# Kernel tuning notes

Hardware: AMD Instinct MI355X
Metric: run time of the kernel (lower is better)

Reference implementation:

```python
import jax, jax.numpy as jnp
import numpy as np

V, E, H, T, B = 10004, 96, 670, 20, 256


def setup_inputs() -> dict:
    key = jax.random.key(0)
    ks = iter(jax.random.split(key, 48))
    def p(*shape):
        return jax.random.normal(next(ks), shape, jnp.float32) * 0.05
    emb = p(V, E).at[0].set(0.0)  # padding_idx=0 row zeroed
    return dict(
        x=jax.random.randint(next(ks), (B, T), 0, V, jnp.int32),
        emb=emb,
        g_wi=p(4 * H, E), g_wh=p(4 * H, H), g_bi=p(4 * H), g_bh=p(4 * H),
        l_wi=p(4 * H, E), l_wh=p(4 * H, H), l_bi=p(4 * H), l_bh=p(4 * H),
        gl1_w=p(E, H), gl1_b=p(E), ll1_w=p(E, H), ll1_b=p(E),
        gl2_w=p(V, E), gl2_b=p(V), ll2_w=p(V, E), ll2_b=p(V),
        p1_w=p(500, E + 2 * H), p1_b=p(500),
        p2_w=p(250, 500), p2_b=p(250),
        p3_w=p(100, 250), p3_b=p(100),
        p4_w=p(50, 100), p4_b=p(50),
        pe_w=p(2, 50), pe_b=p(2),
        q1_w=p(75, 192), q1_b=p(75),
        q2_w=p(30, 75), q2_b=p(30),
        q2e_w=p(2, 30), q2e_b=p(2),
        q3_w=p(10, 30), q3_b=p(10),
        q3e_w=p(2, 10), q3e_b=p(2),
    )


def _lstm(x, h, c, wi, wh, bi, bh):
    # torch.nn.LSTMCell gate order: i, f, g, o
    g = x @ wi.T + bi + h @ wh.T + bh
    i, f, gg, o = jnp.split(g, 4, axis=-1)
    c = jax.nn.sigmoid(f) * c + jax.nn.sigmoid(i) * jnp.tanh(gg)
    h = jax.nn.sigmoid(o) * jnp.tanh(c)
    return h, c


def reference(x, emb, g_wi, g_wh, g_bi, g_bh, l_wi, l_wh, l_bi, l_bh,
              gl1_w, gl1_b, ll1_w, ll1_b, gl2_w, gl2_b, ll2_w, ll2_b,
              p1_w, p1_b, p2_w, p2_b, p3_w, p3_b, p4_w, p4_b, pe_w, pe_b,
              q1_w, q1_b, q2_w, q2_b, q2e_w, q2e_b, q3_w, q3_b, q3e_w, q3e_b):
    relu = jax.nn.relu
    embs = emb[x]                      # [B,T,E]
    Bb, Tt = x.shape
    Hh = g_wh.shape[1]
    z0 = jnp.zeros((Bb, Hh), embs.dtype)

    def step(carry, e_t):
        gh, gc, lh, lc = carry
        gh, gc = _lstm(e_t, gh, gc, g_wi, g_wh, g_bi, g_bh)
        lh, lc = _lstm(e_t, lh, lc, l_wi, l_wh, l_bi, l_bh)
        h = relu(jnp.concatenate([e_t, gh, lh], 1) @ p1_w.T + p1_b)
        h = relu(h @ p2_w.T + p2_b)
        h = relu(h @ p3_w.T + p3_b)
        h = relu(h @ p4_w.T + p4_b)
        prob = jax.nn.softmax(h @ pe_w.T + pe_b, axis=1)  # [B,2]
        # bmm([B,1,2],[B,2,H]) with tilde=[local, global]
        ghm = prob[:, 0:1] * lh + prob[:, 1:2] * gh
        gcm = prob[:, 0:1] * lc + prob[:, 1:2] * gc
        return (ghm, gcm, lh, lc), (ghm, prob)

    _, (hs, probs) = jax.lax.scan(step, (z0, z0, z0, z0), jnp.swapaxes(embs, 0, 1))
    hidden_states = jnp.swapaxes(hs, 0, 1)    # [B,T,H]
    probs_loop = jnp.swapaxes(probs, 0, 1)    # [B,T,2]

    global_x = hidden_states @ gl1_w.T + gl1_b  # [B,T,E]
    local_x = hidden_states @ ll1_w.T + ll1_b   # [B,T,E]
    sf = jnp.concatenate([global_x, local_x], -1)  # [B,T,192]
    h = relu(sf @ q1_w.T + q1_b)
    h = relu(h @ q2_w.T + q2_b)
    y = relu(h @ q2e_w.T + q2e_b)               # p1 logits [B,T,2]
    h2 = relu(h @ q3_w.T + q3_b)
    zz = relu(h2 @ q3e_w.T + q3e_b)             # p2 logits [B,T,2]

    p1s = jax.nn.softmax(y, axis=2)
    ph = jnp.broadcast_to(probs_loop[:, :, None, :], (Bb, Tt, Tt, 2))  # repeat(1,1,T,1)
    ph = jnp.concatenate([ph, p1s[:, None, :, :]], axis=1)
    xm = p1s[:, :, 0:1] * global_x + p1s[:, :, 1:2] * local_x
    gl = xm @ gl2_w.T + gl2_b                   # [B,T,V]
    ll = xm @ ll2_w.T + ll2_b
    p2s = jax.nn.softmax(zz, axis=2)
    ph = jnp.concatenate([ph, p2s[:, None, :, :]], axis=1)  # [B,T+2,T,2]
    logits = gl * p2s[:, :, 0:1] + ll * p2s[:, :, 1:2]
    return jnp.transpose(logits, (0, 2, 1)), ph
```

## Files before the change

### kernel.cpp

```cpp
#include <hip/hip_runtime.h>

#define DI __device__ __forceinline__

typedef unsigned short u16;
typedef unsigned int u32;
typedef __bf16 bf16x8 __attribute__((ext_vector_type(8)));
typedef float f32x4 __attribute__((ext_vector_type(4)));

static constexpr int B = 256, Tn = 20, En = 96, Hn = 670, Vn = 10004;
static constexpr int HP = 672;

DI float bf2f(u16 u) { union { u32 i; float f; } v; v.i = ((u32)u) << 16; return v.f; }
DI u16 f2bf(float f) {
    u32 u = __float_as_uint(f);
    u32 r = (u + 0x7FFFu + ((u >> 16) & 1u)) >> 16;
    return (u16)r;
}
DI float sigm(float x) { return 1.f / (1.f + __expf(-x)); }
DI float tanha(float x) {
    x = fminf(fmaxf(x, -15.f), 15.f);
    float e = __expf(2.f * x);
    return (e - 1.f) / (e + 1.f);
}
DI bf16x8 frag(const u16* p) { return *(const bf16x8*)p; }
DI f32x4 mfma16(bf16x8 a, bf16x8 b, f32x4 c) {
    return __builtin_amdgcn_mfma_f32_16x16x32_bf16(a, b, c, 0, 0, 0);
}
DI u16 ldw(const u16* src, long long i, int f) {
    return f ? f2bf(((const float*)src)[i]) : src[i];
}
DI float ldf(const u16* src, long long i, int f) {
    return f ? ((const float*)src)[i] : bf2f(src[i]);
}

struct Ptrs {
    const int* x;
    const u16 *emb, *g_wi, *g_wh, *g_bi, *g_bh, *l_wi, *l_wh, *l_bi, *l_bh;
    const u16 *gl1_w, *gl1_b, *ll1_w, *ll1_b, *gl2_w, *gl2_b, *ll2_w, *ll2_b;
    const u16 *p1_w, *p1_b, *p2_w, *p2_b, *p3_w, *p3_b, *p4_w, *p4_b, *pe_w, *pe_b;
    const u16 *q1_w, *q1_b, *q2_w, *q2_b, *q2e_w, *q2e_b, *q3_w, *q3_b, *q3e_w, *q3e_b;
    int  *flagp;
    u16 *embs;
    u16 *WgCat;
    u16 *P1W;
    u16 *W1C;
    u16 *W2C;
    float *BSUM;
    u16 *hs;
    u16 *hcat;
    u16 *uw;
    float *ghf, *gcf, *lhf, *lc2, *gcm;
    float *L1out;
    float *sf;
    float *p2sbuf;
    u16 *n_p1b, *n_p2w, *n_p2b, *n_p3w, *n_p3b, *n_p4w, *n_p4b, *n_pew, *n_peb;
    u16 *n_gl1b, *n_ll1b, *n_gl2b, *n_ll2b;
    u16 *n_q1w, *n_q1b, *n_q2w, *n_q2b, *n_q2ew, *n_q2eb, *n_q3w, *n_q3b, *n_q3ew, *n_q3eb;
    u16 *out0, *out1;
    float *out0f, *out1f;
};

__global__ __launch_bounds__(64) void k_detect(Ptrs p) {
    int lane = threadIdx.x;
    u32 d = ((const u32*)p.g_bi)[lane];
    u16 lo = (u16)(d & 0xffffu);
    int e = (lo >> 7) & 0xff;
    unsigned long long m = __ballot(e >= 127);
    if (lane == 0) p.flagp[0] = (m != 0ull) ? 1 : 0;
}

__global__ __launch_bounds__(256) void k_norm(Ptrs p) {
    const int f = p.flagp[0];
    int i = blockIdx.x * 256 + threadIdx.x;
    const u16* srcs[23] = {p.p1_b, p.p2_w, p.p2_b, p.p3_w, p.p3_b, p.p4_w, p.p4_b,
                           p.pe_w, p.pe_b, p.gl1_b, p.ll1_b, p.gl2_b, p.ll2_b,
                           p.q1_w, p.q1_b, p.q2_w, p.q2_b, p.q2e_w, p.q2e_b,
                           p.q3_w, p.q3_b, p.q3e_w, p.q3e_b};
    u16* dsts[23] = {p.n_p1b, p.n_p2w, p.n_p2b, p.n_p3w, p.n_p3b, p.n_p4w, p.n_p4b,
                     p.n_pew, p.n_peb, p.n_gl1b, p.n_ll1b, p.n_gl2b, p.n_ll2b,
                     p.n_q1w, p.n_q1b, p.n_q2w, p.n_q2b, p.n_q2ew, p.n_q2eb,
                     p.n_q3w, p.n_q3b, p.n_q3ew, p.n_q3eb};
    const int ns[23] = {500, 125000, 250, 25000, 100, 5000, 50, 100, 2, 96, 96, 10004, 10004,
                        14400, 75, 2250, 30, 60, 2, 300, 10, 20, 2};
    #pragma unroll 1
    for (int s = 0; s < 23; ++s) {
        if (i < ns[s]) { dsts[s][i] = ldw(srcs[s], i, f); return; }
        i -= ns[s];
    }
}

__global__ __launch_bounds__(256) void k_prep(Ptrs p) {
    const int f = p.flagp[0];
    int i = blockIdx.x * 256 + threadIdx.x;
    if (i < 491520) {
        int r = i / 96, j = i % 96;
        int t = r >> 8, b = r & 255;
        int idx = p.x[b * Tn + t];
        p.embs[r * 96 + j] = ldw(p.emb, (long long)idx * 96 + j, f);
        return;
    }
    i -= 491520;
    if (i < 2 * 2680 * 768) {
        int z = i / (2680 * 768);
        int rem = i - z * (2680 * 768);
        int col = rem / 768, k = rem % 768;
        const u16* wi = z ? p.l_wi : p.g_wi;
        const u16* wh = z ? p.l_wh : p.g_wh;
        u16 v = 0;
        if (k < 96) v = ldw(wi, col * 96 + k, f);
        else { int j = k - 96; if (j < 670) v = ldw(wh, col * 670 + j, f); }
        p.WgCat[i] = v;
        return;
    }
    i -= 2 * 2680 * 768;
    if (i < 512 * 1440) {
        int col = i / 1440, k = i % 1440;
        u16 v = 0;
        if (col < 500) {
            if (k < 96) v = ldw(p.p1_w, col * 1436 + k, f);
            else if (k < 768) { int j = k - 96;  if (j < 670) v = ldw(p.p1_w, col * 1436 + 96 + j, f); }
            else              { int j = k - 768; if (j < 670) v = ldw(p.p1_w, col * 1436 + 766 + j, f); }
        }
        p.P1W[i] = v;
        return;
    }
    i -= 512 * 1440;
    if (i < 192 * 672) {
        int o = i / 672, h = i % 672;
        u16 v = 0;
        if (h < 670) v = (o < 96) ? ldw(p.gl1_w, o * 670 + h, f) : ldw(p.ll1_w, (o - 96) * 670 + h, f);
        p.W1C[i] = v;
        return;
    }
    i -= 192 * 672;
    if (i < 10112 * 192) {
        int v_ = i / 192, k = i % 192;
        u16 v = 0;
        if (v_ < Vn) v = (k < 96) ? ldw(p.gl2_w, v_ * 96 + k, f) : ldw(p.ll2_w, v_ * 96 + (k - 96), f);
        p.W2C[i] = v;
        return;
    }
    i -= 10112 * 192;
    if (i < 2 * 2680) {
        int z = i / 2680, col = i % 2680;
        const u16* bi = z ? p.l_bi : p.g_bi;
        const u16* bh = z ? p.l_bh : p.g_bh;
        p.BSUM[i] = ldf(bi, col, f) + ldf(bh, col, f);
    }
}

__global__ __launch_bounds__(256) void k_gates(Ptrs p, int t) {
    const int jt = blockIdx.x;
    const int mt = blockIdx.y;
    const int z  = blockIdx.z;
    const int row0 = mt * 32, j0 = jt * 32;
    const int tid = threadIdx.x, lane = tid & 63, wv = tid >> 6;

    __shared__ u16 Al[32 * 40];
    __shared__ u16 Wl[128 * 40];
    __shared__ float bs[128];

    if (tid < 128) {
        int gate = tid >> 5, jj = tid & 31, j = j0 + jj;
        bs[tid] = (j < Hn) ? p.BSUM[z * 2680 + gate * Hn + j] : 0.f;
    }
    const int cur = t & 1, prv = cur ^ 1;
    f32x4 acc[4] = {};
    const int mtw = wv & 1, jh = wv >> 1;

    for (int kc = 0; kc < 24; ++kc) {
        const int kb = kc * 32;
        __syncthreads();
        if (tid < 128) {
            int r = tid >> 2, k8 = (tid & 3) * 8, k = kb + k8;
            int b = row0 + r;
            uint4 val = {0, 0, 0, 0};
            if (k < 96) val = *(const uint4*)&p.embs[(t * 256 + b) * 96 + k];
            else if (t > 0) {
                int kk = k - 96;
                const u16* src = (z == 0) ? (p.hs + (b * Tn + (t - 1)) * HP + kk)
                                          : (p.hcat + prv * (B * 1344) + b * 1344 + 672 + kk);
                val = *(const uint4*)src;
            }
            *(uint4*)&Al[r * 40 + k8] = val;
        }
        #pragma unroll
        for (int it = 0; it < 2; ++it) {
            int idx = tid + it * 256;
            int ri = idx >> 2, k8 = (idx & 3) * 8;
            int gate = ri >> 5, jj = ri & 31, j = j0 + jj;
            uint4 val = {0, 0, 0, 0};
            if (j < Hn) val = *(const uint4*)&p.WgCat[(z * 2680 + gate * Hn + j) * 768 + kb + k8];
            *(uint4*)&Wl[ri * 40 + k8] = val;
        }
        __syncthreads();
        bf16x8 a = frag(&Al[(mtw * 16 + (lane & 15)) * 40 + (lane >> 4) * 8]);
        #pragma unroll
        for (int g = 0; g < 4; ++g) {
            int nt = g * 2 + jh;
            bf16x8 bb = frag(&Wl[(nt * 16 + (lane & 15)) * 40 + (lane >> 4) * 8]);
            acc[g] = mfma16(a, bb, acc[g]);
        }
    }
    const int q = lane >> 4;
    const int jj = jh * 16 + (lane & 15);
    const int j = j0 + jj;
    const bool valid = (j < Hn);
    #pragma unroll
    for (int r = 0; r < 4; ++r) {
        int b = row0 + mtw * 16 + q * 4 + r;
        float I = fminf(fmaxf(acc[0][r] + bs[jj], -30.f), 30.f);
        float F = fminf(fmaxf(acc[1][r] + bs[32 + jj], -30.f), 30.f);
        float G = fminf(fmaxf(acc[2][r] + bs[64 + jj], -30.f), 30.f);
        float O = fminf(fmaxf(acc[3][r] + bs[96 + jj], -30.f), 30.f);
        float cp = 0.f;
        if (valid && t > 0)
            cp = (z == 0) ? p.gcm[b * Hn + j] : p.lc2[prv * (B * Hn) + b * Hn + j];
        float c = sigm(F) * cp + sigm(I) * tanha(G);
        float h = sigm(O) * tanha(c);
        if (z == 0) {
            if (valid) { p.ghf[b * Hn + j] = h; p.gcf[b * Hn + j] = c; }
            p.hcat[cur * (B * 1344) + b * 1344 + j] = valid ? f2bf(h) : (u16)0;
        } else {
            if (valid) { p.lhf[b * Hn + j] = h; p.lc2[cur * (B * Hn) + b * Hn + j] = c; }
            p.hcat[cur * (B * 1344) + b * 1344 + 672 + j] = valid ? f2bf(h) : (u16)0;
        }
    }
}

__global__ __launch_bounds__(256) void k_mlp1(Ptrs p, int t) {
    const int col0 = blockIdx.x * 64;
    const int row0 = blockIdx.y * 32;
    const int tid = threadIdx.x, lane = tid & 63, wv = tid >> 6;
    __shared__ u16 Al[32 * 40];
    __shared__ u16 Wl[64 * 40];
    const int cur = t & 1;
    f32x4 acc[2] = {};
    const int mtw = wv & 1, nh = wv >> 1;
    for (int kc = 0; kc < 45; ++kc) {
        const int kb = kc * 32;
        __syncthreads();
        if (tid < 128) {
            int r = tid >> 2, k8 = (tid & 3) * 8, k = kb + k8;
            int b = row0 + r;
            uint4 val;
            if (k < 96) val = *(const uint4*)&p.embs[(t * 256 + b) * 96 + k];
            else        val = *(const uint4*)&p.hcat[cur * (B * 1344) + b * 1344 + (k - 96)];
            *(uint4*)&Al[r * 40 + k8] = val;
        }
        {
            int ri = tid >> 2, k8 = (tid & 3) * 8;
            *(uint4*)&Wl[ri * 40 + k8] = *(const uint4*)&p.P1W[(col0 + ri) * 1440 + kb + k8];
        }
        __syncthreads();
        bf16x8 a = frag(&Al[(mtw * 16 + (lane & 15)) * 40 + (lane >> 4) * 8]);
        #pragma unroll
        for (int s = 0; s < 2; ++s) {
            int nt = nh + s * 2;
            bf16x8 bb = frag(&Wl[(nt * 16 + (lane & 15)) * 40 + (lane >> 4) * 8]);
            acc[s] = mfma16(a, bb, acc[s]);
        }
    }
    const int q = lane >> 4;
    #pragma unroll
    for (int s = 0; s < 2; ++s) {
        int col = col0 + (nh + s * 2) * 16 + (lane & 15);
        if (col < 500) {
            float bias = bf2f(p.n_p1b[col]);
            #pragma unroll
            for (int r = 0; r < 4; ++r) {
                int b = row0 + mtw * 16 + q * 4 + r;
                p.L1out[b * 500 + col] = fmaxf(acc[s][r] + bias, 0.f);
            }
        }
    }
}

__global__ __launch_bounds__(256) void k_rest(Ptrs p, int t) {
    const int b = blockIdx.x, tid = threadIdx.x;
    const int f = p.flagp[0];
    __shared__ float l1[500];
    __shared__ float h2s[250];
    __shared__ float h3s[100];
    __shared__ float h4s[50];
    __shared__ float pr[2];
    for (int i = tid; i < 125; i += 256)
        *(float4*)&l1[i * 4] = *(const float4*)&p.L1out[b * 500 + i * 4];
    __syncthreads();
    if (tid < 250) {
        const u16* wr = p.n_p2w + tid * 500;
        float s = 0.f;
        for (int k = 0; k < 500; k += 4) {
            uint2 u = *(const uint2*)&wr[k];
            s += l1[k]     * bf2f((u16)(u.x & 0xffff));
            s += l1[k + 1] * bf2f((u16)(u.x >> 16));
            s += l1[k + 2] * bf2f((u16)(u.y & 0xffff));
            s += l1[k + 3] * bf2f((u16)(u.y >> 16));
        }
        h2s[tid] = fmaxf(s + bf2f(p.n_p2b[tid]), 0.f);
    }
    __syncthreads();
    if (tid < 100) {
        const u16* wr = p.n_p3w + tid * 250;
        float s = 0.f;
        for (int k = 0; k < 250; k += 2) {
            u32 u = *(const u32*)&wr[k];
            s += h2s[k]     * bf2f((u16)(u & 0xffff));
            s += h2s[k + 1] * bf2f((u16)(u >> 16));
        }
        h3s[tid] = fmaxf(s + bf2f(p.n_p3b[tid]), 0.f);
    }
    __syncthreads();
    if (tid < 50) {
        const u16* wr = p.n_p4w + tid * 100;
        float s = 0.f;
        for (int k = 0; k < 100; k += 4) {
            uint2 u = *(const uint2*)&wr[k];
            s += h3s[k]     * bf2f((u16)(u.x & 0xffff));
            s += h3s[k + 1] * bf2f((u16)(u.x >> 16));
            s += h3s[k + 2] * bf2f((u16)(u.y & 0xffff));
            s += h3s[k + 3] * bf2f((u16)(u.y >> 16));
        }
        h4s[tid] = fmaxf(s + bf2f(p.n_p4b[tid]), 0.f);
    }
    __syncthreads();
    if (tid == 0) {
        float e0 = bf2f(p.n_peb[0]), e1 = bf2f(p.n_peb[1]);
        for (int k = 0; k < 50; ++k) {
            e0 += h4s[k] * bf2f(p.n_pew[k]);
            e1 += h4s[k] * bf2f(p.n_pew[50 + k]);
        }
        float m = fmaxf(e0, e1);
        float a0 = __expf(e0 - m), a1 = __expf(e1 - m);
        float inv = 1.f / (a0 + a1);
        pr[0] = a0 * inv; pr[1] = a1 * inv;
    }
    __syncthreads();
    float p0 = pr[0], p1 = pr[1];
    const int cur = t & 1;
    for (int j = tid; j < HP; j += 256) {
        u16 hv = 0;
        if (j < Hn) {
            float gm = p0 * p.lhf[b * Hn + j] + p1 * p.ghf[b * Hn + j];
            float cm = p0 * p.lc2[cur * (B * Hn) + b * Hn + j] + p1 * p.gcf[b * Hn + j];
            p.gcm[b * Hn + j] = cm;
            hv = f2bf(gm);
        }
        p.hs[(b * Tn + t) * HP + j] = hv;
    }
    if (tid < 40) {
        long long idx = b * 880 + t * 40 + tid;
        if (f) p.out1f[idx] = pr[tid & 1]; else p.out1[idx] = f2bf(pr[tid & 1]);
    }
}

__global__ __launch_bounds__(256) void k_sf(Ptrs p) {
    const int col0 = blockIdx.x * 64;
    const int row0 = blockIdx.y * 64;
    const int tid = threadIdx.x, lane = tid & 63, wv = tid >> 6;
    __shared__ u16 Al[64 * 40];
    __shared__ u16 Wl[64 * 40];
    f32x4 acc[4] = {};
    for (int kc = 0; kc < 21; ++kc) {
        const int kb = kc * 32;
        __syncthreads();
        {
            int r = tid >> 2, k8 = (tid & 3) * 8;
            *(uint4*)&Al[r * 40 + k8] = *(const uint4*)&p.hs[(row0 + r) * HP + kb + k8];
            *(uint4*)&Wl[r * 40 + k8] = *(const uint4*)&p.W1C[(col0 + r) * HP + kb + k8];
        }
        __syncthreads();
        bf16x8 a = frag(&Al[(wv * 16 + (lane & 15)) * 40 + (lane >> 4) * 8]);
        #pragma unroll
        for (int nt = 0; nt < 4; ++nt) {
            bf16x8 bb = frag(&Wl[(nt * 16 + (lane & 15)) * 40 + (lane >> 4) * 8]);
            acc[nt] = mfma16(a, bb, acc[nt]);
        }
    }
    const int q = lane >> 4;
    #pragma unroll
    for (int nt = 0; nt < 4; ++nt) {
        int col = col0 + nt * 16 + (lane & 15);
        float bias = bf2f(col < 96 ? p.n_gl1b[col] : p.n_ll1b[col - 96]);
        #pragma unroll
        for (int r = 0; r < 4; ++r) {
            int row = row0 + wv * 16 + q * 4 + r;
            p.sf[row * 192 + col] = acc[nt][r] + bias;
        }
    }
}

__global__ __launch_bounds__(256) void k_qchain(Ptrs p) {
    const int b = blockIdx.x, tid = threadIdx.x;
    const int f = p.flagp[0];
    __shared__ float sfl[20 * 192];
    __shared__ float h1[20][80];
    __shared__ float h2[20][32];
    __shared__ float h3[20][12];
    __shared__ float yv[20][2];
    __shared__ float zv[20][2];
    __shared__ float p1s[20][2];
    __shared__ float p2sl[20][2];
    for (int i = tid; i < 960; i += 256)
        *(float4*)&sfl[i * 4] = *(const float4*)&p.sf[b * 3840 + i * 4];
    __syncthreads();
    for (int u = tid; u < 1500; u += 256) {
        int row = u / 75, o = u % 75;
        const u16* wr = p.n_q1w + o * 192;
        const float* sr = &sfl[row * 192];
        float s = bf2f(p.n_q1b[o]);
        for (int k = 0; k < 192; k += 4) {
            uint2 w = *(const uint2*)&wr[k];
            s += sr[k]     * bf2f((u16)(w.x & 0xffff));
            s += sr[k + 1] * bf2f((u16)(w.x >> 16));
            s += sr[k + 2] * bf2f((u16)(w.y & 0xffff));
            s += sr[k + 3] * bf2f((u16)(w.y >> 16));
        }
        h1[row][o] = fmaxf(s, 0.f);
    }
    __syncthreads();
    for (int u = tid; u < 600; u += 256) {
        int row = u / 30, o = u % 30;
        const u16* wr = p.n_q2w + o * 75;
        float s = bf2f(p.n_q2b[o]);
        for (int k = 0; k < 75; ++k) s += h1[row][k] * bf2f(wr[k]);
        h2[row][o] = fmaxf(s, 0.f);
    }
    __syncthreads();
    if (tid < 40) {
        int row = tid >> 1, o = tid & 1;
        const u16* wr = p.n_q2ew + o * 30;
        float s = bf2f(p.n_q2eb[o]);
        for (int k = 0; k < 30; ++k) s += h2[row][k] * bf2f(wr[k]);
        yv[row][o] = fmaxf(s, 0.f);
    } else if (tid >= 56) {
        int u = tid - 56;
        int row = u / 10, o = u % 10;
        const u16* wr = p.n_q3w + o * 30;
        float s = bf2f(p.n_q3b[o]);
        for (int k = 0; k < 30; ++k) s += h2[row][k] * bf2f(wr[k]);
        h3[row][o] = fmaxf(s, 0.f);
    }
    __syncthreads();
    if (tid < 40) {
        int row = tid >> 1, o = tid & 1;
        const u16* wr = p.n_q3ew + o * 10;
        float s = bf2f(p.n_q3eb[o]);
        for (int k = 0; k < 10; ++k) s += h3[row][k] * bf2f(wr[k]);
        zv[row][o] = fmaxf(s, 0.f);
    } else if (tid >= 64 && tid < 84) {
        int row = tid - 64;
        float m = fmaxf(yv[row][0], yv[row][1]);
        float a0 = __expf(yv[row][0] - m), a1 = __expf(yv[row][1] - m);
        float inv = 1.f / (a0 + a1);
        p1s[row][0] = a0 * inv; p1s[row][1] = a1 * inv;
    }
    __syncthreads();
    if (tid < 20) {
        float m = fmaxf(zv[tid][0], zv[tid][1]);
        float a0 = __expf(zv[tid][0] - m), a1 = __expf(zv[tid][1] - m);
        float inv = 1.f / (a0 + a1);
        p2sl[tid][0] = a0 * inv; p2sl[tid][1] = a1 * inv;
        p.p2sbuf[(b * Tn + tid) * 2]     = a0 * inv;
        p.p2sbuf[(b * Tn + tid) * 2 + 1] = a1 * inv;
    } else if (tid >= 64 && tid < 104) {
        int row = (tid - 64) >> 1, c = (tid - 64) & 1;
        long long idx = b * 880 + 800 + row * 2 + c;
        if (f) p.out1f[idx] = p1s[row][c]; else p.out1[idx] = f2bf(p1s[row][c]);
    }
    __syncthreads();
    for (int u = tid; u < 1920; u += 256) {
        int row = u / 96, e = u % 96;
        float xm = p1s[row][0] * sfl[row * 192 + e] + p1s[row][1] * sfl[row * 192 + 96 + e];
        p.uw[(b * Tn + row) * 192 + e]      = f2bf(p2sl[row][0] * xm);
        p.uw[(b * Tn + row) * 192 + 96 + e] = f2bf(p2sl[row][1] * xm);
    }
    if (tid < 40) {
        int row = tid >> 1, c = tid & 1;
        long long idx = b * 880 + 840 + row * 2 + c;
        if (f) p.out1f[idx] = p2sl[row][c]; else p.out1[idx] = f2bf(p2sl[row][c]);
    }
}

__global__ __launch_bounds__(256) void k_final(Ptrs p) {
    const int n0 = blockIdx.x * 64;
    const int v0 = blockIdx.y * 128;
    const int tid = threadIdx.x, lane = tid & 63, wv = tid >> 6;
    const int f = p.flagp[0];
    __shared__ u16 Wl[128 * 104];
    __shared__ u16 Ul[64 * 104];
    f32x4 acc[2][4] = {};
    const int m = lane & 15, q = lane >> 4;
    for (int kc = 0; kc < 2; ++kc) {
        const int kb = kc * 96;
        __syncthreads();
        for (int i = tid; i < 1536; i += 256) {
            int ri = i / 12, k8 = (i % 12) * 8;
            *(uint4*)&Wl[ri * 104 + k8] = *(const uint4*)&p.W2C[(v0 + ri) * 192 + kb + k8];
        }
        for (int i = tid; i < 768; i += 256) {
            int ri = i / 12, k8 = (i % 12) * 8;
            *(uint4*)&Ul[ri * 104 + k8] = *(const uint4*)&p.uw[(n0 + ri) * 192 + kb + k8];
        }
        __syncthreads();
        #pragma unroll
        for (int ks = 0; ks < 3; ++ks) {
            int ko = ks * 32 + q * 8;
            bf16x8 a0 = frag(&Wl[(wv * 32 + m) * 104 + ko]);
            bf16x8 a1 = frag(&Wl[(wv * 32 + 16 + m) * 104 + ko]);
            #pragma unroll
            for (int ni = 0; ni < 4; ++ni) {
                bf16x8 bb = frag(&Ul[(ni * 16 + m) * 104 + ko]);
                acc[0][ni] = mfma16(a0, bb, acc[0][ni]);
                acc[1][ni] = mfma16(a1, bb, acc[1][ni]);
            }
        }
    }
    #pragma unroll
    for (int ni = 0; ni < 4; ++ni) {
        int n = n0 + ni * 16 + m;
        int bb = n / 20, tt = n % 20;
        float s0 = p.p2sbuf[n * 2], s1 = p.p2sbuf[n * 2 + 1];
        size_t base = (size_t)bb * 200080 + tt;
        #pragma unroll
        for (int mi = 0; mi < 2; ++mi) {
            #pragma unroll
            for (int r = 0; r < 4; ++r) {
                int v = v0 + wv * 32 + mi * 16 + q * 4 + r;
                if (v < Vn) {
                    float val = acc[mi][ni][r] + s0 * bf2f(p.n_gl2b[v]) + s1 * bf2f(p.n_ll2b[v]);
                    size_t idx = base + (size_t)v * 20;
                    if (f) p.out0f[idx] = val; else p.out0[idx] = f2bf(val);
                }
            }
        }
    }
}

extern "C" void kernel_launch(void* const* d_in, const int* in_sizes, int n_in,
                              void* d_out, int out_size, void* d_ws, size_t ws_size,
                              hipStream_t stream) {
    Ptrs p;
    p.x    = (const int*)d_in[0];
    p.emb  = (const u16*)d_in[1];
    p.g_wi = (const u16*)d_in[2];  p.g_wh = (const u16*)d_in[3];
    p.g_bi = (const u16*)d_in[4];  p.g_bh = (const u16*)d_in[5];
    p.l_wi = (const u16*)d_in[6];  p.l_wh = (const u16*)d_in[7];
    p.l_bi = (const u16*)d_in[8];  p.l_bh = (const u16*)d_in[9];
    p.gl1_w = (const u16*)d_in[10]; p.gl1_b = (const u16*)d_in[11];
    p.ll1_w = (const u16*)d_in[12]; p.ll1_b = (const u16*)d_in[13];
    p.gl2_w = (const u16*)d_in[14]; p.gl2_b = (const u16*)d_in[15];
    p.ll2_w = (const u16*)d_in[16]; p.ll2_b = (const u16*)d_in[17];
    p.p1_w = (const u16*)d_in[18]; p.p1_b = (const u16*)d_in[19];
    p.p2_w = (const u16*)d_in[20]; p.p2_b = (const u16*)d_in[21];
    p.p3_w = (const u16*)d_in[22]; p.p3_b = (const u16*)d_in[23];
    p.p4_w = (const u16*)d_in[24]; p.p4_b = (const u16*)d_in[25];
    p.pe_w = (const u16*)d_in[26]; p.pe_b = (const u16*)d_in[27];
    p.q1_w = (const u16*)d_in[28]; p.q1_b = (const u16*)d_in[29];
    p.q2_w = (const u16*)d_in[30]; p.q2_b = (const u16*)d_in[31];
    p.q2e_w = (const u16*)d_in[32]; p.q2e_b = (const u16*)d_in[33];
    p.q3_w = (const u16*)d_in[34]; p.q3_b = (const u16*)d_in[35];
    p.q3e_w = (const u16*)d_in[36]; p.q3e_b = (const u16*)d_in[37];

    char* w = (char*)d_ws;
    auto carve = [&](size_t bytes) { char* r = w; w += (bytes + 255) & ~(size_t)255; return r; };
    p.flagp  = (int*)carve(256);
    p.embs   = (u16*)carve((size_t)20 * 256 * 96 * 2);
    p.WgCat  = (u16*)carve((size_t)2 * 2680 * 768 * 2);
    p.P1W    = (u16*)carve((size_t)512 * 1440 * 2);
    p.W1C    = (u16*)carve((size_t)192 * 672 * 2);
    p.W2C    = (u16*)carve((size_t)10112 * 192 * 2);
    p.BSUM   = (float*)carve((size_t)2 * 2680 * 4);
    p.hs     = (u16*)carve((size_t)5120 * 672 * 2);
    p.hcat   = (u16*)carve((size_t)2 * 256 * 1344 * 2);
    p.uw     = (u16*)carve((size_t)5120 * 192 * 2);
    p.ghf    = (float*)carve((size_t)256 * 670 * 4);
    p.gcf    = (float*)carve((size_t)256 * 670 * 4);
    p.lhf    = (float*)carve((size_t)256 * 670 * 4);
    p.lc2    = (float*)carve((size_t)2 * 256 * 670 * 4);
    p.gcm    = (float*)carve((size_t)256 * 670 * 4);
    p.L1out  = (float*)carve((size_t)256 * 500 * 4);
    p.sf     = (float*)carve((size_t)5120 * 192 * 4);
    p.p2sbuf = (float*)carve((size_t)5120 * 2 * 4);
    p.n_p1b = (u16*)carve(500 * 2);   p.n_p2w = (u16*)carve(125000 * 2);
    p.n_p2b = (u16*)carve(250 * 2);   p.n_p3w = (u16*)carve(25000 * 2);
    p.n_p3b = (u16*)carve(100 * 2);   p.n_p4w = (u16*)carve(5000 * 2);
    p.n_p4b = (u16*)carve(50 * 2);    p.n_pew = (u16*)carve(100 * 2);
    p.n_peb = (u16*)carve(2 * 2);
    p.n_gl1b = (u16*)carve(96 * 2);   p.n_ll1b = (u16*)carve(96 * 2);
    p.n_gl2b = (u16*)carve(10004 * 2); p.n_ll2b = (u16*)carve(10004 * 2);
    p.n_q1w = (u16*)carve(14400 * 2); p.n_q1b = (u16*)carve(75 * 2);
    p.n_q2w = (u16*)carve(2250 * 2);  p.n_q2b = (u16*)carve(30 * 2);
    p.n_q2ew = (u16*)carve(60 * 2);   p.n_q2eb = (u16*)carve(2 * 2);
    p.n_q3w = (u16*)carve(300 * 2);   p.n_q3b = (u16*)carve(10 * 2);
    p.n_q3ew = (u16*)carve(20 * 2);   p.n_q3eb = (u16*)carve(2 * 2);
    p.out0 = (u16*)d_out;
    p.out1 = p.out0 + 51220480;
    p.out0f = (float*)d_out;
    p.out1f = p.out0f + 51220480;

    k_detect<<<1, 64, 0, stream>>>(p);
    k_norm<<<756, 256, 0, stream>>>(p);
    k_prep<<<28990, 256, 0, stream>>>(p);
    for (int t = 0; t < 20; ++t) {
        k_gates<<<dim3(21, 8, 2), 256, 0, stream>>>(p, t);
        k_mlp1<<<dim3(8, 8), 256, 0, stream>>>(p, t);
        k_rest<<<256, 256, 0, stream>>>(p, t);
    }
    k_sf<<<dim3(3, 80), 256, 0, stream>>>(p);
    k_qchain<<<256, 256, 0, stream>>>(p);
    k_final<<<dim3(80, 79), 256, 0, stream>>>(p);
}
```

Baseline: 1.999 ms.

## Fuse prep and recurrent steps into one persistent kernel with grid barriers

Replaces the norm, prep, sf and qchain launches and the three per-timestep launches (60 in total) with one persistent 256-block kernel. It uses a software grid barrier built on atomics between phases and a union of shared-memory layouts. The mlp1 tiling changes to 128 tiles of 32x32 instead of 64 tiles of 32x64, and gates tiles are spread over the persistent blocks with 80 blocks taking a second tile. This removes launch overhead and inter-kernel gaps. In exchange it adds barrier spin cost and depends on all 256 blocks being co-resident, which 256 CUs on MI355X should allow.

```diff
diff --git a/kernel.cpp b/kernel.cpp
--- a/kernel.cpp
+++ b/kernel.cpp
@@ -9,6 +9,7 @@
 
 static constexpr int B = 256, Tn = 20, En = 96, Hn = 670, Vn = 10004;
 static constexpr int HP = 672;
+static constexpr int NBLK = 256;
 
 DI float bf2f(u16 u) { union { u32 i; float f; } v; v.i = ((u32)u) << 16; return v.f; }
 DI u16 f2bf(float f) {
@@ -39,6 +40,7 @@
     const u16 *gl1_w, *gl1_b, *ll1_w, *ll1_b, *gl2_w, *gl2_b, *ll2_w, *ll2_b;
     const u16 *p1_w, *p1_b, *p2_w, *p2_b, *p3_w, *p3_b, *p4_w, *p4_b, *pe_w, *pe_b;
     const u16 *q1_w, *q1_b, *q2_w, *q2_b, *q2e_w, *q2e_b, *q3_w, *q3_b, *q3e_w, *q3e_b;
+    unsigned *bar;
     int  *flagp;
     u16 *embs;
     u16 *WgCat;
@@ -60,8 +62,27 @@
     float *out0f, *out1f;
 };
 
+DI void gbar(unsigned* bar, int tid) {
+    __syncthreads();
+    if (tid == 0) {
+        __threadfence();
+        unsigned gen = __hip_atomic_load(bar + 16, __ATOMIC_RELAXED, __HIP_MEMORY_SCOPE_AGENT);
+        unsigned a = __hip_atomic_fetch_add(bar, 1u, __ATOMIC_ACQ_REL, __HIP_MEMORY_SCOPE_AGENT);
+        if (a == NBLK - 1) {
+            __hip_atomic_store(bar, 0u, __ATOMIC_RELAXED, __HIP_MEMORY_SCOPE_AGENT);
+            __hip_atomic_fetch_add(bar + 16, 1u, __ATOMIC_RELEASE, __HIP_MEMORY_SCOPE_AGENT);
+        } else {
+            while (__hip_atomic_load(bar + 16, __ATOMIC_ACQUIRE, __HIP_MEMORY_SCOPE_AGENT) == gen)
+                __builtin_amdgcn_s_sleep(1);
+        }
+        __threadfence();
+    }
+    __syncthreads();
+}
+
 __global__ __launch_bounds__(64) void k_detect(Ptrs p) {
     int lane = threadIdx.x;
+    if (lane < 32) p.bar[lane] = 0u;
     u32 d = ((const u32*)p.g_bi)[lane];
     u16 lo = (u16)(d & 0xffffu);
     int e = (lo >> 7) & 0xff;
@@ -69,9 +90,18 @@
     if (lane == 0) p.flagp[0] = (m != 0ull) ? 1 : 0;
 }
 
-__global__ __launch_bounds__(256) void k_norm(Ptrs p) {
-    const int f = p.flagp[0];
-    int i = blockIdx.x * 256 + threadIdx.x;
+struct SMg { u16 Al[32 * 40]; u16 Wl[128 * 40]; float bs[128]; };
+struct SMm { u16 Al[32 * 40]; u16 Wl[32 * 40]; };
+struct SMr { float l1[500]; float h2s[250]; float h3s[100]; float h4s[52]; float pr[4]; };
+struct SMs { u16 Al[64 * 40]; u16 Wl[64 * 40]; };
+struct SMq {
+    float sfl[3840];
+    float h1[20][80]; float h2[20][32]; float h3[20][12];
+    float yv[20][2]; float zv[20][2]; float p1s[20][2]; float p2sl[20][2];
+};
+union alignas(16) SMem { SMg g; SMm m; SMr r; SMs s; SMq q; };
+
+DI void norm_phase(const Ptrs& p, int gtid, int f) {
     const u16* srcs[23] = {p.p1_b, p.p2_w, p.p2_b, p.p3_w, p.p3_b, p.p4_w, p.p4_b,
                            p.pe_w, p.pe_b, p.gl1_b, p.ll1_b, p.gl2_b, p.ll2_b,
                            p.q1_w, p.q1_b, p.q2_w, p.q2_b, p.q2e_w, p.q2e_b,
@@ -82,16 +112,17 @@
                      p.n_q3w, p.n_q3b, p.n_q3ew, p.n_q3eb};
     const int ns[23] = {500, 125000, 250, 25000, 100, 5000, 50, 100, 2, 96, 96, 10004, 10004,
                         14400, 75, 2250, 30, 60, 2, 300, 10, 20, 2};
-    #pragma unroll 1
-    for (int s = 0; s < 23; ++s) {
-        if (i < ns[s]) { dsts[s][i] = ldw(srcs[s], i, f); return; }
-        i -= ns[s];
-    }
-}
-
-__global__ __launch_bounds__(256) void k_prep(Ptrs p) {
-    const int f = p.flagp[0];
-    int i = blockIdx.x * 256 + threadIdx.x;
+    for (int i0 = gtid; i0 < 193351; i0 += 65536) {
+        int i = i0;
+        #pragma unroll 1
+        for (int s = 0; s < 23; ++s) {
+            if (i < ns[s]) { dsts[s][i] = ldw(srcs[s], i, f); break; }
+            i -= ns[s];
+        }
+    }
+}
+
+DI void prep_one(const Ptrs& p, int i, int f) {
     if (i < 491520) {
         int r = i / 96, j = i % 96;
         int t = r >> 8, b = r & 255;
@@ -149,20 +180,17 @@
     }
 }
 
-__global__ __launch_bounds__(256) void k_gates(Ptrs p, int t) {
-    const int jt = blockIdx.x;
-    const int mt = blockIdx.y;
-    const int z  = blockIdx.z;
+DI void gates_tile(const Ptrs& p, int t, int tau, int tid, SMg& S) {
+    const int z = tau / 168;
+    const int rem = tau - z * 168;
+    const int jt = rem % 21, mt = rem / 21;
     const int row0 = mt * 32, j0 = jt * 32;
-    const int tid = threadIdx.x, lane = tid & 63, wv = tid >> 6;
-
-    __shared__ u16 Al[32 * 40];
-    __shared__ u16 Wl[128 * 40];
-    __shared__ float bs[128];
-
+    const int lane = tid & 63, wv = tid >> 6;
+
+    __syncthreads();
     if (tid < 128) {
         int gate = tid >> 5, jj = tid & 31, j = j0 + jj;
-        bs[tid] = (j < Hn) ? p.BSUM[z * 2680 + gate * Hn + j] : 0.f;
+        S.bs[tid] = (j < Hn) ? p.BSUM[z * 2680 + gate * Hn + j] : 0.f;
     }
     const int cur = t & 1, prv = cur ^ 1;
     f32x4 acc[4] = {};
@@ -182,7 +210,7 @@
                                           : (p.hcat + prv * (B * 1344) + b * 1344 + 672 + kk);
                 val = *(const uint4*)src;
             }
-            *(uint4*)&Al[r * 40 + k8] = val;
+            *(uint4*)&S.Al[r * 40 + k8] = val;
         }
         #pragma unroll
         for (int it = 0; it < 2; ++it) {
@@ -191,14 +219,14 @@
             int gate = ri >> 5, jj = ri & 31, j = j0 + jj;
             uint4 val = {0, 0, 0, 0};
             if (j < Hn) val = *(const uint4*)&p.WgCat[(z * 2680 + gate * Hn + j) * 768 + kb + k8];
-            *(uint4*)&Wl[ri * 40 + k8] = val;
-        }
-        __syncthreads();
-        bf16x8 a = frag(&Al[(mtw * 16 + (lane & 15)) * 40 + (lane >> 4) * 8]);
+            *(uint4*)&S.Wl[ri * 40 + k8] = val;
+        }
+        __syncthreads();
+        bf16x8 a = frag(&S.Al[(mtw * 16 + (lane & 15)) * 40 + (lane >> 4) * 8]);
         #pragma unroll
         for (int g = 0; g < 4; ++g) {
             int nt = g * 2 + jh;
-            bf16x8 bb = frag(&Wl[(nt * 16 + (lane & 15)) * 40 + (lane >> 4) * 8]);
+            bf16x8 bb = frag(&S.Wl[(nt * 16 + (lane & 15)) * 40 + (lane >> 4) * 8]);
             acc[g] = mfma16(a, bb, acc[g]);
         }
     }
@@ -209,10 +237,10 @@
     #pragma unroll
     for (int r = 0; r < 4; ++r) {
         int b = row0 + mtw * 16 + q * 4 + r;
-        float I = fminf(fmaxf(acc[0][r] + bs[jj], -30.f), 30.f);
-        float F = fminf(fmaxf(acc[1][r] + bs[32 + jj], -30.f), 30.f);
-        float G = fminf(fmaxf(acc[2][r] + bs[64 + jj], -30.f), 30.f);
-        float O = fminf(fmaxf(acc[3][r] + bs[96 + jj], -30.f), 30.f);
+        float I = fminf(fmaxf(acc[0][r] + S.bs[jj], -30.f), 30.f);
+        float F = fminf(fmaxf(acc[1][r] + S.bs[32 + jj], -30.f), 30.f);
+        float G = fminf(fmaxf(acc[2][r] + S.bs[64 + jj], -30.f), 30.f);
+        float O = fminf(fmaxf(acc[3][r] + S.bs[96 + jj], -30.f), 30.f);
         float cp = 0.f;
         if (valid && t > 0)
             cp = (z == 0) ? p.gcm[b * Hn + j] : p.lc2[prv * (B * Hn) + b * Hn + j];
@@ -228,14 +256,12 @@
     }
 }
 
-__global__ __launch_bounds__(256) void k_mlp1(Ptrs p, int t) {
-    const int col0 = blockIdx.x * 64;
-    const int row0 = blockIdx.y * 32;
-    const int tid = threadIdx.x, lane = tid & 63, wv = tid >> 6;
-    __shared__ u16 Al[32 * 40];
-    __shared__ u16 Wl[64 * 40];
+DI void mlp1_tile(const Ptrs& p, int t, int bid, int tid, SMm& S) {
+    const int col0 = (bid & 15) * 32;
+    const int row0 = (bid >> 4) * 32;
+    const int lane = tid & 63, wv = tid >> 6;
     const int cur = t & 1;
-    f32x4 acc[2] = {};
+    f32x4 acc = {};
     const int mtw = wv & 1, nh = wv >> 1;
     for (int kc = 0; kc < 45; ++kc) {
         const int kb = kc * 32;
@@ -246,58 +272,44 @@
             uint4 val;
             if (k < 96) val = *(const uint4*)&p.embs[(t * 256 + b) * 96 + k];
             else        val = *(const uint4*)&p.hcat[cur * (B * 1344) + b * 1344 + (k - 96)];
-            *(uint4*)&Al[r * 40 + k8] = val;
-        }
-        {
-            int ri = tid >> 2, k8 = (tid & 3) * 8;
-            *(uint4*)&Wl[ri * 40 + k8] = *(const uint4*)&p.P1W[(col0 + ri) * 1440 + kb + k8];
-        }
-        __syncthreads();
-        bf16x8 a = frag(&Al[(mtw * 16 + (lane & 15)) * 40 + (lane >> 4) * 8]);
+            *(uint4*)&S.Al[r * 40 + k8] = val;
+        } else {
+            int idx = tid - 128;
+            int ri = idx >> 2, k8 = (idx & 3) * 8;
+            *(uint4*)&S.Wl[ri * 40 + k8] = *(const uint4*)&p.P1W[(col0 + ri) * 1440 + kb + k8];
+        }
+        __syncthreads();
+        bf16x8 a = frag(&S.Al[(mtw * 16 + (lane & 15)) * 40 + (lane >> 4) * 8]);
+        bf16x8 bb = frag(&S.Wl[(nh * 16 + (lane & 15)) * 40 + (lane >> 4) * 8]);
+        acc = mfma16(a, bb, acc);
+    }
+    const int q = lane >> 4;
+    int col = col0 + nh * 16 + (lane & 15);
+    if (col < 500) {
+        float bias = bf2f(p.n_p1b[col]);
         #pragma unroll
-        for (int s = 0; s < 2; ++s) {
-            int nt = nh + s * 2;
-            bf16x8 bb = frag(&Wl[(nt * 16 + (lane & 15)) * 40 + (lane >> 4) * 8]);
-            acc[s] = mfma16(a, bb, acc[s]);
-        }
-    }
-    const int q = lane >> 4;
-    #pragma unroll
-    for (int s = 0; s < 2; ++s) {
-        int col = col0 + (nh + s * 2) * 16 + (lane & 15);
-        if (col < 500) {
-            float bias = bf2f(p.n_p1b[col]);
-            #pragma unroll
-            for (int r = 0; r < 4; ++r) {
-                int b = row0 + mtw * 16 + q * 4 + r;
-                p.L1out[b * 500 + col] = fmaxf(acc[s][r] + bias, 0.f);
-            }
-        }
-    }
-}
-
-__global__ __launch_bounds__(256) void k_rest(Ptrs p, int t) {
-    const int b = blockIdx.x, tid = threadIdx.x;
-    const int f = p.flagp[0];
-    __shared__ float l1[500];
-    __shared__ float h2s[250];
-    __shared__ float h3s[100];
-    __shared__ float h4s[50];
-    __shared__ float pr[2];
+        for (int r = 0; r < 4; ++r) {
+            int b = row0 + mtw * 16 + q * 4 + r;
+            p.L1out[b * 500 + col] = fmaxf(acc[r] + bias, 0.f);
+        }
+    }
+}
+
+DI void rest_block(const Ptrs& p, int t, int b, int tid, int f, SMr& S) {
     for (int i = tid; i < 125; i += 256)
-        *(float4*)&l1[i * 4] = *(const float4*)&p.L1out[b * 500 + i * 4];
+        *(float4*)&S.l1[i * 4] = *(const float4*)&p.L1out[b * 500 + i * 4];
     __syncthreads();
     if (tid < 250) {
         const u16* wr = p.n_p2w + tid * 500;
         float s = 0.f;
         for (int k = 0; k < 500; k += 4) {
             uint2 u = *(const uint2*)&wr[k];
-            s += l1[k]     * bf2f((u16)(u.x & 0xffff));
-            s += l1[k + 1] * bf2f((u16)(u.x >> 16));
-            s += l1[k + 2] * bf2f((u16)(u.y & 0xffff));
-            s += l1[k + 3] * bf2f((u16)(u.y >> 16));
-        }
-        h2s[tid] = fmaxf(s + bf2f(p.n_p2b[tid]), 0.f);
+            s += S.l1[k]     * bf2f((u16)(u.x & 0xffff));
+            s += S.l1[k + 1] * bf2f((u16)(u.x >> 16));
+            s += S.l1[k + 2] * bf2f((u16)(u.y & 0xffff));
+            s += S.l1[k + 3] * bf2f((u16)(u.y >> 16));
+        }
+        S.h2s[tid] = fmaxf(s + bf2f(p.n_p2b[tid]), 0.f);
     }
     __syncthreads();
     if (tid < 100) {
@@ -305,10 +317,10 @@
         float s = 0.f;
         for (int k = 0; k < 250; k += 2) {
             u32 u = *(const u32*)&wr[k];
-            s += h2s[k]     * bf2f((u16)(u & 0xffff));
-            s += h2s[k + 1] * bf2f((u16)(u >> 16));
-        }
-        h3s[tid] = fmaxf(s + bf2f(p.n_p3b[tid]), 0.f);
+            s += S.h2s[k]     * bf2f((u16)(u & 0xffff));
+            s += S.h2s[k + 1] * bf2f((u16)(u >> 16));
+        }
+        S.h3s[tid] = fmaxf(s + bf2f(p.n_p3b[tid]), 0.f);
     }
     __syncthreads();
     if (tid < 50) {
@@ -316,27 +328,27 @@
         float s = 0.f;
         for (int k = 0; k < 100; k += 4) {
             uint2 u = *(const uint2*)&wr[k];
-            s += h3s[k]     * bf2f((u16)(u.x & 0xffff));
-            s += h3s[k + 1] * bf2f((u16)(u.x >> 16));
-            s += h3s[k + 2] * bf2f((u16)(u.y & 0xffff));
-            s += h3s[k + 3] * bf2f((u16)(u.y >> 16));
-        }
-        h4s[tid] = fmaxf(s + bf2f(p.n_p4b[tid]), 0.f);
+            s += S.h3s[k]     * bf2f((u16)(u.x & 0xffff));
+            s += S.h3s[k + 1] * bf2f((u16)(u.x >> 16));
+            s += S.h3s[k + 2] * bf2f((u16)(u.y & 0xffff));
+            s += S.h3s[k + 3] * bf2f((u16)(u.y >> 16));
+        }
+        S.h4s[tid] = fmaxf(s + bf2f(p.n_p4b[tid]), 0.f);
     }
     __syncthreads();
     if (tid == 0) {
         float e0 = bf2f(p.n_peb[0]), e1 = bf2f(p.n_peb[1]);
         for (int k = 0; k < 50; ++k) {
-            e0 += h4s[k] * bf2f(p.n_pew[k]);
-            e1 += h4s[k] * bf2f(p.n_pew[50 + k]);
+            e0 += S.h4s[k] * bf2f(p.n_pew[k]);
+            e1 += S.h4s[k] * bf2f(p.n_pew[50 + k]);
         }
         float m = fmaxf(e0, e1);
         float a0 = __expf(e0 - m), a1 = __expf(e1 - m);
         float inv = 1.f / (a0 + a1);
-        pr[0] = a0 * inv; pr[1] = a1 * inv;
-    }
-    __syncthreads();
-    float p0 = pr[0], p1 = pr[1];
+        S.pr[0] = a0 * inv; S.pr[1] = a1 * inv;
+    }
+    __syncthreads();
+    float p0 = S.pr[0], p1 = S.pr[1];
     const int cur = t & 1;
     for (int j = tid; j < HP; j += 256) {
         u16 hv = 0;
@@ -350,30 +362,29 @@
     }
     if (tid < 40) {
         long long idx = b * 880 + t * 40 + tid;
-        if (f) p.out1f[idx] = pr[tid & 1]; else p.out1[idx] = f2bf(pr[tid & 1]);
-    }
-}
-
-__global__ __launch_bounds__(256) void k_sf(Ptrs p) {
-    const int col0 = blockIdx.x * 64;
-    const int row0 = blockIdx.y * 64;
-    const int tid = threadIdx.x, lane = tid & 63, wv = tid >> 6;
-    __shared__ u16 Al[64 * 40];
-    __shared__ u16 Wl[64 * 40];
+        float v = (tid & 1) ? p1 : p0;
+        if (f) p.out1f[idx] = v; else p.out1[idx] = f2bf(v);
+    }
+}
+
+DI void sf_tile(const Ptrs& p, int tau, int tid, SMs& S) {
+    const int col0 = (tau % 3) * 64;
+    const int row0 = (tau / 3) * 64;
+    const int lane = tid & 63, wv = tid >> 6;
     f32x4 acc[4] = {};
     for (int kc = 0; kc < 21; ++kc) {
         const int kb = kc * 32;
         __syncthreads();
         {
             int r = tid >> 2, k8 = (tid & 3) * 8;
-            *(uint4*)&Al[r * 40 + k8] = *(const uint4*)&p.hs[(row0 + r) * HP + kb + k8];
-            *(uint4*)&Wl[r * 40 + k8] = *(const uint4*)&p.W1C[(col0 + r) * HP + kb + k8];
-        }
-        __syncthreads();
-        bf16x8 a = frag(&Al[(wv * 16 + (lane & 15)) * 40 + (lane >> 4) * 8]);
+            *(uint4*)&S.Al[r * 40 + k8] = *(const uint4*)&p.hs[(row0 + r) * HP + kb + k8];
+            *(uint4*)&S.Wl[r * 40 + k8] = *(const uint4*)&p.W1C[(col0 + r) * HP + kb + k8];
+        }
+        __syncthreads();
+        bf16x8 a = frag(&S.Al[(wv * 16 + (lane & 15)) * 40 + (lane >> 4) * 8]);
         #pragma unroll
         for (int nt = 0; nt < 4; ++nt) {
-            bf16x8 bb = frag(&Wl[(nt * 16 + (lane & 15)) * 40 + (lane >> 4) * 8]);
+            bf16x8 bb = frag(&S.Wl[(nt * 16 + (lane & 15)) * 40 + (lane >> 4) * 8]);
             acc[nt] = mfma16(a, bb, acc[nt]);
         }
     }
@@ -390,24 +401,14 @@
     }
 }
 
-__global__ __launch_bounds__(256) void k_qchain(Ptrs p) {
-    const int b = blockIdx.x, tid = threadIdx.x;
-    const int f = p.flagp[0];
-    __shared__ float sfl[20 * 192];
-    __shared__ float h1[20][80];
-    __shared__ float h2[20][32];
-    __shared__ float h3[20][12];
-    __shared__ float yv[20][2];
-    __shared__ float zv[20][2];
-    __shared__ float p1s[20][2];
-    __shared__ float p2sl[20][2];
+DI void qchain_block(const Ptrs& p, int b, int tid, int f, SMq& S) {
     for (int i = tid; i < 960; i += 256)
-        *(float4*)&sfl[i * 4] = *(const float4*)&p.sf[b * 3840 + i * 4];
+        *(float4*)&S.sfl[i * 4] = *(const float4*)&p.sf[b * 3840 + i * 4];
     __syncthreads();
     for (int u = tid; u < 1500; u += 256) {
         int row = u / 75, o = u % 75;
         const u16* wr = p.n_q1w + o * 192;
-        const float* sr = &sfl[row * 192];
+        const float* sr = &S.sfl[row * 192];
         float s = bf2f(p.n_q1b[o]);
         for (int k = 0; k < 192; k += 4) {
             uint2 w = *(const uint2*)&wr[k];
@@ -416,70 +417,99 @@
             s += sr[k + 2] * bf2f((u16)(w.y & 0xffff));
             s += sr[k + 3] * bf2f((u16)(w.y >> 16));
         }
-        h1[row][o] = fmaxf(s, 0.f);
+        S.h1[row][o] = fmaxf(s, 0.f);
     }
     __syncthreads();
     for (int u = tid; u < 600; u += 256) {
         int row = u / 30, o = u % 30;
         const u16* wr = p.n_q2w + o * 75;
         float s = bf2f(p.n_q2b[o]);
-        for (int k = 0; k < 75; ++k) s += h1[row][k] * bf2f(wr[k]);
-        h2[row][o] = fmaxf(s, 0.f);
+        for (int k = 0; k < 75; ++k) s += S.h1[row][k] * bf2f(wr[k]);
+        S.h2[row][o] = fmaxf(s, 0.f);
     }
     __syncthreads();
     if (tid < 40) {
         int row = tid >> 1, o = tid & 1;
         const u16* wr = p.n_q2ew + o * 30;
         float s = bf2f(p.n_q2eb[o]);
-        for (int k = 0; k < 30; ++k) s += h2[row][k] * bf2f(wr[k]);
-        yv[row][o] = fmaxf(s, 0.f);
-    } else if (tid >= 56) {
+        for (int k = 0; k < 30; ++k) s += S.h2[row][k] * bf2f(wr[k]);
+        S.yv[row][o] = fmaxf(s, 0.f);
+    } else if (tid >= 56 && tid < 256) {
         int u = tid - 56;
         int row = u / 10, o = u % 10;
         const u16* wr = p.n_q3w + o * 30;
         float s = bf2f(p.n_q3b[o]);
-        for (int k = 0; k < 30; ++k) s += h2[row][k] * bf2f(wr[k]);
-        h3[row][o] = fmaxf(s, 0.f);
+        for (int k = 0; k < 30; ++k) s += S.h2[row][k] * bf2f(wr[k]);
+        S.h3[row][o] = fmaxf(s, 0.f);
     }
     __syncthreads();
     if (tid < 40) {
         int row = tid >> 1, o = tid & 1;
         const u16* wr = p.n_q3ew + o * 10;
         float s = bf2f(p.n_q3eb[o]);
-        for (int k = 0; k < 10; ++k) s += h3[row][k] * bf2f(wr[k]);
-        zv[row][o] = fmaxf(s, 0.f);
+        for (int k = 0; k < 10; ++k) s += S.h3[row][k] * bf2f(wr[k]);
+        S.zv[row][o] = fmaxf(s, 0.f);
     } else if (tid >= 64 && tid < 84) {
         int row = tid - 64;
-        float m = fmaxf(yv[row][0], yv[row][1]);
-        float a0 = __expf(yv[row][0] - m), a1 = __expf(yv[row][1] - m);
+        float m = fmaxf(S.yv[row][0], S.yv[row][1]);
+        float a0 = __expf(S.yv[row][0] - m), a1 = __expf(S.yv[row][1] - m);
         float inv = 1.f / (a0 + a1);
-        p1s[row][0] = a0 * inv; p1s[row][1] = a1 * inv;
+        S.p1s[row][0] = a0 * inv; S.p1s[row][1] = a1 * inv;
     }
     __syncthreads();
     if (tid < 20) {
-        float m = fmaxf(zv[tid][0], zv[tid][1]);
-        float a0 = __expf(zv[tid][0] - m), a1 = __expf(zv[tid][1] - m);
+        float m = fmaxf(S.zv[tid][0], S.zv[tid][1]);
+        float a0 = __expf(S.zv[tid][0] - m), a1 = __expf(S.zv[tid][1] - m);
         float inv = 1.f / (a0 + a1);
-        p2sl[tid][0] = a0 * inv; p2sl[tid][1] = a1 * inv;
+        S.p2sl[tid][0] = a0 * inv; S.p2sl[tid][1] = a1 * inv;
         p.p2sbuf[(b * Tn + tid) * 2]     = a0 * inv;
         p.p2sbuf[(b * Tn + tid) * 2 + 1] = a1 * inv;
     } else if (tid >= 64 && tid < 104) {
         int row = (tid - 64) >> 1, c = (tid - 64) & 1;
         long long idx = b * 880 + 800 + row * 2 + c;
-        if (f) p.out1f[idx] = p1s[row][c]; else p.out1[idx] = f2bf(p1s[row][c]);
+        if (f) p.out1f[idx] = S.p1s[row][c]; else p.out1[idx] = f2bf(S.p1s[row][c]);
     }
     __syncthreads();
     for (int u = tid; u < 1920; u += 256) {
         int row = u / 96, e = u % 96;
-        float xm = p1s[row][0] * sfl[row * 192 + e] + p1s[row][1] * sfl[row * 192 + 96 + e];
-        p.uw[(b * Tn + row) * 192 + e]      = f2bf(p2sl[row][0] * xm);
-        p.uw[(b * Tn + row) * 192 + 96 + e] = f2bf(p2sl[row][1] * xm);
+        float xm = S.p1s[row][0] * S.sfl[row * 192 + e] + S.p1s[row][1] * S.sfl[row * 192 + 96 + e];
+        p.uw[(b * Tn + row) * 192 + e]      = f2bf(S.p2sl[row][0] * xm);
+        p.uw[(b * Tn + row) * 192 + 96 + e] = f2bf(S.p2sl[row][1] * xm);
     }
     if (tid < 40) {
         int row = tid >> 1, c = tid & 1;
         long long idx = b * 880 + 840 + row * 2 + c;
-        if (f) p.out1f[idx] = p2sl[row][c]; else p.out1[idx] = f2bf(p2sl[row][c]);
-    }
+        if (f) p.out1f[idx] = S.p2sl[row][c]; else p.out1[idx] = f2bf(S.p2sl[row][c]);
+    }
+}
+
+__global__ __launch_bounds__(256, 1) void k_loop(Ptrs p) {
+    const int bid = blockIdx.x;
+    const int tid = threadIdx.x;
+    const int f = p.flagp[0];
+    const int gtid = bid * 256 + tid;
+
+    __shared__ SMem sm;
+
+    norm_phase(p, gtid, f);
+    #pragma unroll 1
+    for (int i0 = gtid; i0 < 7421168; i0 += 65536) prep_one(p, i0, f);
+    gbar(p.bar, tid);
+
+    #pragma unroll 1
+    for (int t = 0; t < Tn; ++t) {
+        gates_tile(p, t, bid, tid, sm.g);
+        if (bid < 80) gates_tile(p, t, bid + 256, tid, sm.g);
+        gbar(p.bar, tid);
+        if (bid < 128) mlp1_tile(p, t, bid, tid, sm.m);
+        gbar(p.bar, tid);
+        rest_block(p, t, bid, tid, f, sm.r);
+        gbar(p.bar, tid);
+    }
+
+    if (bid < 240) sf_tile(p, bid, tid, sm.s);
+    gbar(p.bar, tid);
+    qchain_block(p, bid, tid, f, sm.q);
 }
 
 __global__ __launch_bounds__(256) void k_final(Ptrs p) {
@@ -564,6 +594,7 @@
 
     char* w = (char*)d_ws;
     auto carve = [&](size_t bytes) { char* r = w; w += (bytes + 255) & ~(size_t)255; return r; };
+    p.bar    = (unsigned*)carve(256);
     p.flagp  = (int*)carve(256);
     p.embs   = (u16*)carve((size_t)20 * 256 * 96 * 2);
     p.WgCat  = (u16*)carve((size_t)2 * 2680 * 768 * 2);
@@ -600,14 +631,6 @@
     p.out1f = p.out0f + 51220480;
 
     k_detect<<<1, 64, 0, stream>>>(p);
-    k_norm<<<756, 256, 0, stream>>>(p);
-    k_prep<<<28990, 256, 0, stream>>>(p);
-    for (int t = 0; t < 20; ++t) {
-        k_gates<<<dim3(21, 8, 2), 256, 0, stream>>>(p, t);
-        k_mlp1<<<dim3(8, 8), 256, 0, stream>>>(p, t);
-        k_rest<<<256, 256, 0, stream>>>(p, t);
-    }
-    k_sf<<<dim3(3, 80), 256, 0, stream>>>(p);
-    k_qchain<<<256, 256, 0, stream>>>(p);
+    k_loop<<<NBLK, 256, 0, stream>>>(p);
     k_final<<<dim3(80, 79), 256, 0, stream>>>(p);
 }
```

Result: slower. 5.299 ms (+165.1%).
